# Optimization experiments

Measured on AMD Instinct MI355X. Metric: run time of the kernel, lower is better.

The kernel has to match this reference:

```python
import jax, jax.numpy as jnp
import numpy as np

# Model config (matches init_kwargs)
B, T, D = 2, 2048, 2048
H, KH, F = 16, 4, 8192
HD = D // H            # 128
G = H // KH            # q heads per kv head = 4
EPS = 1e-5


def _ln(x, g, b):
    m = jnp.mean(x, axis=-1, keepdims=True)
    v = jnp.mean((x - m) ** 2, axis=-1, keepdims=True)
    return (x - m) * jax.lax.rsqrt(v + EPS) * g + b


def setup_inputs() -> dict:
    key = jax.random.key(0)
    ks = jax.random.split(key, 8)

    def xav(k, shape):
        lim = (6.0 / (shape[0] + shape[1])) ** 0.5
        return jax.random.uniform(k, shape, jnp.float32, -lim, lim)

    x = jax.random.normal(ks[0], (B, T, D), jnp.float32)
    mask = jnp.tril(jnp.ones((1, 1, T, T), jnp.int32))  # causal
    # Linear weights stored as [in, out] (transpose of torch nn.Linear)
    return {
        "x": x,
        "mask": mask,
        "Wq": xav(ks[1], (D, H * HD)), "bq": jnp.zeros((H * HD,), jnp.float32),
        "Wk": xav(ks[2], (D, KH * HD)), "bk": jnp.zeros((KH * HD,), jnp.float32),
        "Wv": xav(ks[3], (D, KH * HD)), "bv": jnp.zeros((KH * HD,), jnp.float32),
        "Wo": xav(ks[4], (H * HD, D)), "bo": jnp.zeros((D,), jnp.float32),
        "ln1_g": jnp.ones((D,), jnp.float32), "ln1_b": jnp.zeros((D,), jnp.float32),
        "ln2_g": jnp.ones((D,), jnp.float32), "ln2_b": jnp.zeros((D,), jnp.float32),
        "fln_g": jnp.ones((D,), jnp.float32), "fln_b": jnp.zeros((D,), jnp.float32),
        "W1": xav(ks[5], (D, F)), "b1": jnp.zeros((F,), jnp.float32),
        "W2": xav(ks[6], (D, F)), "b2": jnp.zeros((F,), jnp.float32),
        "W3": xav(ks[7], (F, D)), "b3": jnp.zeros((D,), jnp.float32),
    }


def reference(x, mask, Wq, bq, Wk, bk, Wv, bv, Wo, bo,
              ln1_g, ln1_b, ln2_g, ln2_b, fln_g, fln_b,
              W1, b1, W2, b2, W3, b3):
    scale = 1.0 / np.sqrt(HD)
    # --- attention block (pre-LN + residual) ---
    h = _ln(x, ln1_g, ln1_b)
    q = (h @ Wq + bq).reshape(B, T, KH, G, HD)   # q head k*G+g uses kv head k
    k = (h @ Wk + bk).reshape(B, T, KH, HD)
    v = (h @ Wv + bv).reshape(B, T, KH, HD)
    # GQA scores without repeat_interleave: broadcast kv head across group g
    scores = jnp.einsum('btkgd,bskd->bkgts', q, k) * scale  # [B,KH,G,T,T]
    scores = jnp.clip(scores, -100.0, 100.0)
    scores = jnp.where(mask[:, :, None] == 0, -jnp.inf, scores)
    attn = jax.nn.softmax(scores, axis=-1)
    ctx = jnp.einsum('bkgts,bskd->btkgd', attn, v).reshape(B, T, H * HD)
    x = x + (ctx @ Wo + bo)  # dropout is identity in eval
    # --- ln2 then SwiGLU FFN (which has its own internal LN and residual
    # around the *post-ln2* activation, faithful to original) ---
    x = _ln(x, ln2_g, ln2_b)
    r = x
    h2 = _ln(x, fln_g, fln_b)
    g_pre = h2 @ W1 + b1
    gate = g_pre * jax.nn.sigmoid(jnp.clip(g_pre, -10.0, 10.0))
    hidden = h2 @ W2 + b2
    return r + ((gate * hidden) @ W3 + b3)
```

## Files before the change

kernel.cpp:

```cpp
#include <hip/hip_runtime.h>
#include <math.h>
#include <stdint.h>

typedef __bf16 bf16_t;
typedef __bf16 bf16x4 __attribute__((ext_vector_type(4)));
typedef __bf16 bf16x8 __attribute__((ext_vector_type(8)));
typedef float  f32x4  __attribute__((ext_vector_type(4)));

#define D_MODEL 2048
#define T_SEQ   2048
#define BATCH   2
#define NROWS   (BATCH*T_SEQ)
#define NHEAD   16
#define HDIM    128
#define KVH     4
#define KVD     (KVH*HDIM)
#define FDIM    8192
#define QKVN    3072

__device__ __forceinline__ bf16x8 mk8(bf16x4 lo, bf16x4 hi) {
  union { bf16x4 h[2]; bf16x8 v; } u;
  u.h[0] = lo; u.h[1] = hi; return u.v;
}

__device__ __forceinline__ void gl16(const bf16_t* g, bf16_t* l) {
  __builtin_amdgcn_global_load_lds(
      (const uint32_t __attribute__((address_space(1)))*)g,
      (uint32_t __attribute__((address_space(3)))*)l, 16, 0, 0);
}

__global__ __launch_bounds__(256)
void transpose_w(const float* __restrict__ in, bf16_t* __restrict__ outT, int K, int N)
{
  __shared__ __align__(16) bf16_t t[64][72];
  const int tid = threadIdx.x;
  const int k0 = blockIdx.y * 64, n0 = blockIdx.x * 64;
  const int tr = tid >> 4, tc = (tid & 15) * 4;
#pragma unroll
  for (int i = 0; i < 4; ++i) {
    f32x4 v = *(const f32x4*)(in + (size_t)(k0 + tr + 16 * i) * N + n0 + tc);
#pragma unroll
    for (int e = 0; e < 4; ++e) t[tr + 16 * i][tc + e] = (bf16_t)v[e];
  }
  __syncthreads();
#pragma unroll
  for (int s = 0; s < 2; ++s) {
    const int c = s * 256 + tid;
    const int n = c >> 3, c8 = (c & 7) * 8;
    bf16x8 o;
#pragma unroll
    for (int e = 0; e < 8; ++e) o[e] = t[c8 + e][n];
    *(bf16x8*)(outT + (size_t)(n0 + n) * K + k0 + c8) = o;
  }
}

__global__ __launch_bounds__(256)
void concat_bias(const float* __restrict__ a, const float* __restrict__ b,
                 const float* __restrict__ c, float* __restrict__ dst)
{
  const int i = blockIdx.x * 256 + threadIdx.x;
  if (i >= QKVN) return;
  dst[i] = (i < 2048) ? a[i] : (i < 2560) ? b[i - 2048] : c[i - 2560];
}

template<typename TI>
__global__ __launch_bounds__(256)
void ln_kernel(const TI* __restrict__ x, const float* __restrict__ g,
               const float* __restrict__ b, bf16_t* __restrict__ out)
{
  const int row = blockIdx.x;
  const int tid = threadIdx.x;
  const TI* xr = x + (size_t)row * D_MODEL;
  float vals[8];
  if constexpr (sizeof(TI) == 4) {
    f32x4 v0 = *(const f32x4*)(xr + tid * 8);
    f32x4 v1 = *(const f32x4*)(xr + tid * 8 + 4);
#pragma unroll
    for (int e = 0; e < 4; ++e) { vals[e] = v0[e]; vals[4 + e] = v1[e]; }
  } else {
    bf16x8 v = *(const bf16x8*)(xr + tid * 8);
#pragma unroll
    for (int e = 0; e < 8; ++e) vals[e] = (float)v[e];
  }
  float s = 0.f, s2 = 0.f;
#pragma unroll
  for (int e = 0; e < 8; ++e) { s += vals[e]; s2 += vals[e] * vals[e]; }
#pragma unroll
  for (int off = 1; off < 64; off <<= 1) { s += __shfl_xor(s, off); s2 += __shfl_xor(s2, off); }
  __shared__ float red[8];
  const int wid = tid >> 6, lane = tid & 63;
  if (lane == 0) { red[wid] = s; red[4 + wid] = s2; }
  __syncthreads();
  s  = red[0] + red[1] + red[2] + red[3];
  s2 = red[4] + red[5] + red[6] + red[7];
  const float mean = s * (1.f / D_MODEL);
  const float var  = s2 * (1.f / D_MODEL) - mean * mean;
  const float rstd = rsqrtf(var + 1e-5f);
  f32x4 g0 = *(const f32x4*)(g + tid * 8), g1 = *(const f32x4*)(g + tid * 8 + 4);
  f32x4 b0 = *(const f32x4*)(b + tid * 8), b1 = *(const f32x4*)(b + tid * 8 + 4);
  bf16x8 o;
#pragma unroll
  for (int e = 0; e < 4; ++e) {
    o[e]     = (bf16_t)((vals[e]     - mean) * rstd * g0[e] + b0[e]);
    o[4 + e] = (bf16_t)((vals[4 + e] - mean) * rstd * g1[e] + b1[e]);
  }
  *(bf16x8*)(out + (size_t)row * D_MODEL + tid * 8) = o;
}

__global__ __launch_bounds__(256)
void ln2_fused(const bf16_t* __restrict__ x, const float* __restrict__ g2,
               const float* __restrict__ b2, const float* __restrict__ gf,
               const float* __restrict__ bf_, bf16_t* __restrict__ rout,
               bf16_t* __restrict__ hout)
{
  const int row = blockIdx.x;
  const int tid = threadIdx.x;
  const int wid = tid >> 6, lane = tid & 63;
  __shared__ float red[8];
  const bf16_t* xr = x + (size_t)row * D_MODEL;
  bf16x8 v = *(const bf16x8*)(xr + tid * 8);
  float vals[8]; float s = 0.f, s2 = 0.f;
#pragma unroll
  for (int e = 0; e < 8; ++e) { vals[e] = (float)v[e]; s += vals[e]; s2 += vals[e] * vals[e]; }
#pragma unroll
  for (int off = 1; off < 64; off <<= 1) { s += __shfl_xor(s, off); s2 += __shfl_xor(s2, off); }
  if (lane == 0) { red[wid] = s; red[4 + wid] = s2; }
  __syncthreads();
  s  = red[0] + red[1] + red[2] + red[3];
  s2 = red[4] + red[5] + red[6] + red[7];
  float mean = s * (1.f / D_MODEL);
  float var  = s2 * (1.f / D_MODEL) - mean * mean;
  float rstd = rsqrtf(var + 1e-5f);
  f32x4 ga0 = *(const f32x4*)(g2 + tid * 8), ga1 = *(const f32x4*)(g2 + tid * 8 + 4);
  f32x4 ba0 = *(const f32x4*)(b2 + tid * 8), ba1 = *(const f32x4*)(b2 + tid * 8 + 4);
  float y[8];
#pragma unroll
  for (int e = 0; e < 4; ++e) {
    y[e]     = (vals[e]     - mean) * rstd * ga0[e] + ba0[e];
    y[4 + e] = (vals[4 + e] - mean) * rstd * ga1[e] + ba1[e];
  }
  bf16x8 o1;
#pragma unroll
  for (int e = 0; e < 8; ++e) o1[e] = (bf16_t)y[e];
  *(bf16x8*)(rout + (size_t)row * D_MODEL + tid * 8) = o1;
  s = 0.f; s2 = 0.f;
#pragma unroll
  for (int e = 0; e < 8; ++e) { s += y[e]; s2 += y[e] * y[e]; }
#pragma unroll
  for (int off = 1; off < 64; off <<= 1) { s += __shfl_xor(s, off); s2 += __shfl_xor(s2, off); }
  __syncthreads();
  if (lane == 0) { red[wid] = s; red[4 + wid] = s2; }
  __syncthreads();
  s  = red[0] + red[1] + red[2] + red[3];
  s2 = red[4] + red[5] + red[6] + red[7];
  mean = s * (1.f / D_MODEL);
  var  = s2 * (1.f / D_MODEL) - mean * mean;
  rstd = rsqrtf(var + 1e-5f);
  f32x4 gb0 = *(const f32x4*)(gf + tid * 8), gb1 = *(const f32x4*)(gf + tid * 8 + 4);
  f32x4 bb0 = *(const f32x4*)(bf_ + tid * 8), bb1 = *(const f32x4*)(bf_ + tid * 8 + 4);
  bf16x8 o2;
#pragma unroll
  for (int e = 0; e < 4; ++e) {
    o2[e]     = (bf16_t)((y[e]     - mean) * rstd * gb0[e] + bb0[e]);
    o2[4 + e] = (bf16_t)((y[4 + e] - mean) * rstd * gb1[e] + bb1[e]);
  }
  *(bf16x8*)(hout + (size_t)row * D_MODEL + tid * 8) = o2;
}

enum { EPI_NONE = 0, EPI_RES = 1, EPI_SILU = 2, EPI_MUL = 3 };

__device__ __forceinline__ void xcd_swz(int BMv, int BNv, int& m0, int& n0) {
  const int nbx = gridDim.x, nwg = nbx * gridDim.y;
  int flat = blockIdx.y * nbx + blockIdx.x;
  flat = (flat & 7) * (nwg >> 3) + (flat >> 3);
  m0 = (flat / nbx) * BMv; n0 = (flat % nbx) * BNv;
}

template<int EPI, int BM_T, typename TE, typename TO>
__global__ __launch_bounds__(512, 2)
void gemm8p(const bf16_t* __restrict__ A, const bf16_t* __restrict__ Bt,
            const float* __restrict__ bias, const TE* __restrict__ extra,
            TO* __restrict__ out, int M, int N, int K)
{
  constexpr int ALs = BM_T / 128;
  constexpr int RF  = BM_T / 32;
  __shared__ __align__(16) bf16_t As[2][2][BM_T * 32];
  __shared__ __align__(16) bf16_t Bs[2][2][256 * 32];
  const int tid = threadIdx.x, lane = tid & 63, wid = tid >> 6;
  const int wr = wid >> 2, wc = wid & 3;
  const int l16 = lane & 15, lq = lane >> 4;
  int m0, n0; xcd_swz(BM_T, 256, m0, n0);

  const bf16_t* aP[ALs]; int aL[ALs];
#pragma unroll
  for (int s = 0; s < ALs; ++s) {
    const int c = s * 512 + tid;
    const int row = c >> 2, pos = c & 3;
    aP[s] = A + (size_t)(m0 + row) * K + (pos ^ ((row >> 1) & 3)) * 8;
    aL[s] = (s * 512 + wid * 64) * 8;
  }
  const bf16_t* bP[2]; int bL[2];
#pragma unroll
  for (int s = 0; s < 2; ++s) {
    const int c = s * 512 + tid;
    const int row = c >> 2, pos = c & 3;
    bP[s] = Bt + (size_t)(n0 + row) * K + (pos ^ ((row >> 1) & 3)) * 8;
    bL[s] = (s * 512 + wid * 64) * 8;
  }

  int offA[RF];
#pragma unroll
  for (int i = 0; i < RF; ++i) {
    const int r = wr * (BM_T / 2) + i * 16 + l16;
    offA[i] = r * 32 + ((lq ^ ((r >> 1) & 3)) * 8);
  }
  int offB[4];
#pragma unroll
  for (int jj = 0; jj < 4; ++jj) {
    const int r = wc * 64 + jj * 16 + l16;
    offB[jj] = r * 32 + ((lq ^ ((r >> 1) & 3)) * 8);
  }

  f32x4 acc[RF][4];
#pragma unroll
  for (int i = 0; i < RF; ++i)
#pragma unroll
    for (int j = 0; j < 4; ++j) acc[i][j] = (f32x4){0.f, 0.f, 0.f, 0.f};

  auto SA = [&](int t, int bb, int kh) {
#pragma unroll
    for (int s = 0; s < ALs; ++s) gl16(aP[s] + t * 64 + kh * 32, &As[bb][kh][aL[s]]);
  };
  auto SB = [&](int t, int bb, int kh) {
#pragma unroll
    for (int s = 0; s < 2; ++s) gl16(bP[s] + t * 64 + kh * 32, &Bs[bb][kh][bL[s]]);
  };
#define BAR_()  __builtin_amdgcn_s_barrier()
#define LGKM_() do { asm volatile("s_waitcnt lgkmcnt(0)" ::: "memory"); \
                     __builtin_amdgcn_sched_barrier(0); } while (0)

  const int nt = K >> 6;
  SA(0, 0, 0); SB(0, 0, 0); SA(0, 0, 1); SB(0, 0, 1);
  if (nt > 1) { SA(1, 1, 0); SB(1, 1, 0); SA(1, 1, 1); }
  if (nt > 2) {
    if constexpr (ALs == 2) asm volatile("s_waitcnt vmcnt(6)" ::: "memory");
    else                    asm volatile("s_waitcnt vmcnt(4)" ::: "memory");
  } else {
    asm volatile("s_waitcnt vmcnt(0)" ::: "memory");
  }
  BAR_();

  for (int t = 0; t < nt; ++t) {
    const int b = t & 1, ob = b ^ 1;
    const bool s1 = (t + 1 < nt), s2 = (t + 2 < nt);
    bf16x8 af[RF], bf0, bf1;
#pragma unroll
    for (int i = 0; i < RF; ++i) af[i] = *(const bf16x8*)(&As[b][0][offA[i]]);
    bf0 = *(const bf16x8*)(&Bs[b][0][offB[0]]);
    bf1 = *(const bf16x8*)(&Bs[b][0][offB[1]]);
    if (s1) SB(t + 1, ob, 1);
    BAR_(); LGKM_();
    __builtin_amdgcn_s_setprio(1);
#pragma unroll
    for (int i = 0; i < RF; ++i) {
      acc[i][0] = __builtin_amdgcn_mfma_f32_16x16x32_bf16(af[i], bf0, acc[i][0], 0, 0, 0);
      acc[i][1] = __builtin_amdgcn_mfma_f32_16x16x32_bf16(af[i], bf1, acc[i][1], 0, 0, 0);
    }
    __builtin_amdgcn_s_setprio(0);
    BAR_();
    bf0 = *(const bf16x8*)(&Bs[b][0][offB[2]]);
    bf1 = *(const bf16x8*)(&Bs[b][0][offB[3]]);
    if (s2) SA(t + 2, b, 0);
    BAR_(); LGKM_();
    __builtin_amdgcn_s_setprio(1);
#pragma unroll
    for (int i = 0; i < RF; ++i) {
      acc[i][2] = __builtin_amdgcn_mfma_f32_16x16x32_bf16(af[i], bf0, acc[i][2], 0, 0, 0);
      acc[i][3] = __builtin_amdgcn_mfma_f32_16x16x32_bf16(af[i], bf1, acc[i][3], 0, 0, 0);
    }
    __builtin_amdgcn_s_setprio(0);
    BAR_();
#pragma unroll
    for (int i = 0; i < RF; ++i) af[i] = *(const bf16x8*)(&As[b][1][offA[i]]);
    bf0 = *(const bf16x8*)(&Bs[b][1][offB[0]]);
    bf1 = *(const bf16x8*)(&Bs[b][1][offB[1]]);
    if (s2) SB(t + 2, b, 0);
    BAR_(); LGKM_();
    __builtin_amdgcn_s_setprio(1);
#pragma unroll
    for (int i = 0; i < RF; ++i) {
      acc[i][0] = __builtin_amdgcn_mfma_f32_16x16x32_bf16(af[i], bf0, acc[i][0], 0, 0, 0);
      acc[i][1] = __builtin_amdgcn_mfma_f32_16x16x32_bf16(af[i], bf1, acc[i][1], 0, 0, 0);
    }
    __builtin_amdgcn_s_setprio(0);
    BAR_();
    bf0 = *(const bf16x8*)(&Bs[b][1][offB[2]]);
    bf1 = *(const bf16x8*)(&Bs[b][1][offB[3]]);
    if (s2) SA(t + 2, b, 1);
    BAR_(); LGKM_();
    __builtin_amdgcn_s_setprio(1);
#pragma unroll
    for (int i = 0; i < RF; ++i) {
      acc[i][2] = __builtin_amdgcn_mfma_f32_16x16x32_bf16(af[i], bf0, acc[i][2], 0, 0, 0);
      acc[i][3] = __builtin_amdgcn_mfma_f32_16x16x32_bf16(af[i], bf1, acc[i][3], 0, 0, 0);
    }
    __builtin_amdgcn_s_setprio(0);
    if (t < nt - 2) {
      if constexpr (ALs == 2) asm volatile("s_waitcnt vmcnt(6)" ::: "memory");
      else                    asm volatile("s_waitcnt vmcnt(4)" ::: "memory");
    } else {
      asm volatile("s_waitcnt vmcnt(0)" ::: "memory");
    }
    BAR_();
  }

  if constexpr (sizeof(TO) == 2) {
    float* sc = (float*)(&As[0][0][0]) + (size_t)wid * (16 * 72);
    const int rr = lane >> 3, cc8 = (lane & 7) * 8;
#pragma unroll
    for (int i = 0; i < RF; ++i) {
      const int row0 = m0 + wr * (BM_T / 2) + i * 16;
#pragma unroll
      for (int j = 0; j < 4; ++j) {
        const float bb = bias[n0 + wc * 64 + j * 16 + l16];
#pragma unroll
        for (int e = 0; e < 4; ++e) {
          float vv = acc[i][j][e] + bb;
          if (EPI == EPI_SILU) { float c2 = fminf(fmaxf(vv, -10.f), 10.f); vv = vv / (1.f + __expf(-c2)); }
          sc[(lq * 4 + e) * 72 + j * 16 + l16] = vv;
        }
      }
      asm volatile("s_waitcnt lgkmcnt(0)" ::: "memory");
      __builtin_amdgcn_sched_barrier(0);
#pragma unroll
      for (int q = 0; q < 2; ++q) {
        const int row = row0 + rr + q * 8;
        const size_t base = (size_t)row * N + n0 + wc * 64 + cc8;
        f32x4 a0 = *(const f32x4*)(sc + (rr + q * 8) * 72 + cc8);
        f32x4 a1 = *(const f32x4*)(sc + (rr + q * 8) * 72 + cc8 + 4);
        bf16x8 o;
        if constexpr (EPI == EPI_RES) {
          if constexpr (sizeof(TE) == 4) {
            f32x4 x0 = *(const f32x4*)((const float*)extra + base);
            f32x4 x1 = *(const f32x4*)((const float*)extra + base + 4);
#pragma unroll
            for (int e = 0; e < 4; ++e) { o[e] = (bf16_t)(a0[e] + x0[e]); o[4 + e] = (bf16_t)(a1[e] + x1[e]); }
          } else {
            bf16x8 x8 = *(const bf16x8*)((const bf16_t*)extra + base);
#pragma unroll
            for (int e = 0; e < 4; ++e) { o[e] = (bf16_t)(a0[e] + (float)x8[e]); o[4 + e] = (bf16_t)(a1[e] + (float)x8[4 + e]); }
          }
        } else if constexpr (EPI == EPI_MUL) {
          bf16x8 x8 = *(const bf16x8*)((const bf16_t*)extra + base);
#pragma unroll
          for (int e = 0; e < 4; ++e) { o[e] = (bf16_t)(a0[e] * (float)x8[e]); o[4 + e] = (bf16_t)(a1[e] * (float)x8[4 + e]); }
        } else {
#pragma unroll
          for (int e = 0; e < 4; ++e) { o[e] = (bf16_t)a0[e]; o[4 + e] = (bf16_t)a1[e]; }
        }
        *(bf16x8*)((bf16_t*)out + base) = o;
      }
      asm volatile("s_waitcnt lgkmcnt(0)" ::: "memory");
      __builtin_amdgcn_sched_barrier(0);
    }
  } else {
#pragma unroll
    for (int j = 0; j < 4; ++j) {
      const int col = n0 + wc * 64 + j * 16 + l16;
      const float bb = bias[col];
#pragma unroll
      for (int i = 0; i < RF; ++i) {
        const int row0 = m0 + wr * (BM_T / 2) + i * 16 + lq * 4;
#pragma unroll
        for (int e = 0; e < 4; ++e) {
          const size_t idx = (size_t)(row0 + e) * N + col;
          float vv = acc[i][j][e] + bb;
          if (EPI == EPI_RES)       vv += (float)extra[idx];
          else if (EPI == EPI_SILU) { float c2 = fminf(fmaxf(vv, -10.f), 10.f); vv = vv / (1.f + __expf(-c2)); }
          else if (EPI == EPI_MUL)  vv *= (float)extra[idx];
          out[idx] = (TO)vv;
        }
      }
    }
  }
#undef BAR_
#undef LGKM_
}

template<int EPI, typename TE, typename TO>
__global__ __launch_bounds__(256, 4)
void gemm3b(const bf16_t* __restrict__ A, const bf16_t* __restrict__ Bt,
            const float* __restrict__ bias, const TE* __restrict__ extra,
            TO* __restrict__ out, int M, int N, int K)
{
  __shared__ __align__(16) bf16_t As[3][128 * 32];
  __shared__ __align__(16) bf16_t Bs[3][128 * 32];
  const int tid = threadIdx.x, lane = tid & 63, wid = tid >> 6;
  const int wr = wid >> 1, wc = wid & 1;
  const int l16 = lane & 15, lq = lane >> 4;
  int m0, n0; xcd_swz(128, 128, m0, n0);

  const bf16_t* aP[2]; const bf16_t* bP[2]; int sL[2];
#pragma unroll
  for (int s = 0; s < 2; ++s) {
    const int c = s * 256 + tid;
    const int row = c >> 2, pos = c & 3;
    const int g = pos ^ ((row >> 1) & 3);
    aP[s] = A  + (size_t)(m0 + row) * K + g * 8;
    bP[s] = Bt + (size_t)(n0 + row) * K + g * 8;
    sL[s] = (s * 256 + wid * 64) * 8;
  }

  int offA[4], offB[4];
#pragma unroll
  for (int i = 0; i < 4; ++i) {
    const int r = wr * 64 + i * 16 + l16;
    offA[i] = r * 32 + ((lq ^ ((r >> 1) & 3)) * 8);
  }
#pragma unroll
  for (int j = 0; j < 4; ++j) {
    const int r = wc * 64 + j * 16 + l16;
    offB[j] = r * 32 + ((lq ^ ((r >> 1) & 3)) * 8);
  }

  f32x4 acc[4][4];
#pragma unroll
  for (int i = 0; i < 4; ++i)
#pragma unroll
    for (int j = 0; j < 4; ++j) acc[i][j] = (f32x4){0.f, 0.f, 0.f, 0.f};

  auto STAGE = [&](int t, int b) {
    gl16(aP[0] + t * 32, &As[b][sL[0]]);
    gl16(aP[1] + t * 32, &As[b][sL[1]]);
    gl16(bP[0] + t * 32, &Bs[b][sL[0]]);
    gl16(bP[1] + t * 32, &Bs[b][sL[1]]);
  };

  const int nt = K >> 5;
  STAGE(0, 0);
  STAGE(1, 1);
  if (nt > 1) asm volatile("s_waitcnt vmcnt(4)" ::: "memory");
  else        asm volatile("s_waitcnt vmcnt(0)" ::: "memory");
  __builtin_amdgcn_s_barrier();

  int b = 0;
  for (int t = 0; t < nt; ++t) {
    bf16x8 af[4], bfr[4];
#pragma unroll
    for (int i = 0; i < 4; ++i) af[i]  = *(const bf16x8*)(&As[b][offA[i]]);
#pragma unroll
    for (int j = 0; j < 4; ++j) bfr[j] = *(const bf16x8*)(&Bs[b][offB[j]]);
    if (t + 2 < nt) {
      STAGE(t + 2, (b + 2) % 3);
      asm volatile("s_waitcnt vmcnt(4)" ::: "memory");
    } else {
      asm volatile("s_waitcnt vmcnt(0)" ::: "memory");
    }
    __builtin_amdgcn_s_barrier();
    asm volatile("s_waitcnt lgkmcnt(0)" ::: "memory");
    __builtin_amdgcn_sched_barrier(0);
    __builtin_amdgcn_s_setprio(1);
#pragma unroll
    for (int i = 0; i < 4; ++i)
#pragma unroll
      for (int j = 0; j < 4; ++j)
        acc[i][j] = __builtin_amdgcn_mfma_f32_16x16x32_bf16(af[i], bfr[j], acc[i][j], 0, 0, 0);
    __builtin_amdgcn_s_setprio(0);
    __builtin_amdgcn_s_barrier();
    b = (b + 1) % 3;
  }

  if constexpr (sizeof(TO) == 2) {
    float* sc = (float*)(&As[0][0]) + (size_t)wid * (16 * 72);
    const int rr = lane >> 3, cc8 = (lane & 7) * 8;
#pragma unroll
    for (int i = 0; i < 4; ++i) {
      const int row0 = m0 + wr * 64 + i * 16;
#pragma unroll
      for (int j = 0; j < 4; ++j) {
        const float bb = bias[n0 + wc * 64 + j * 16 + l16];
#pragma unroll
        for (int e = 0; e < 4; ++e) {
          float vv = acc[i][j][e] + bb;
          if (EPI == EPI_SILU) { float c2 = fminf(fmaxf(vv, -10.f), 10.f); vv = vv / (1.f + __expf(-c2)); }
          sc[(lq * 4 + e) * 72 + j * 16 + l16] = vv;
        }
      }
      asm volatile("s_waitcnt lgkmcnt(0)" ::: "memory");
      __builtin_amdgcn_sched_barrier(0);
#pragma unroll
      for (int q = 0; q < 2; ++q) {
        const int row = row0 + rr + q * 8;
        const size_t base = (size_t)row * N + n0 + wc * 64 + cc8;
        f32x4 a0 = *(const f32x4*)(sc + (rr + q * 8) * 72 + cc8);
        f32x4 a1 = *(const f32x4*)(sc + (rr + q * 8) * 72 + cc8 + 4);
        bf16x8 o;
        if constexpr (EPI == EPI_RES) {
          if constexpr (sizeof(TE) == 4) {
            f32x4 x0 = *(const f32x4*)((const float*)extra + base);
            f32x4 x1 = *(const f32x4*)((const float*)extra + base + 4);
#pragma unroll
            for (int e = 0; e < 4; ++e) { o[e] = (bf16_t)(a0[e] + x0[e]); o[4 + e] = (bf16_t)(a1[e] + x1[e]); }
          } else {
            bf16x8 x8 = *(const bf16x8*)((const bf16_t*)extra + base);
#pragma unroll
            for (int e = 0; e < 4; ++e) { o[e] = (bf16_t)(a0[e] + (float)x8[e]); o[4 + e] = (bf16_t)(a1[e] + (float)x8[4 + e]); }
          }
        } else if constexpr (EPI == EPI_MUL) {
          bf16x8 x8 = *(const bf16x8*)((const bf16_t*)extra + base);
#pragma unroll
          for (int e = 0; e < 4; ++e) { o[e] = (bf16_t)(a0[e] * (float)x8[e]); o[4 + e] = (bf16_t)(a1[e] * (float)x8[4 + e]); }
        } else {
#pragma unroll
          for (int e = 0; e < 4; ++e) { o[e] = (bf16_t)a0[e]; o[4 + e] = (bf16_t)a1[e]; }
        }
        *(bf16x8*)((bf16_t*)out + base) = o;
      }
      asm volatile("s_waitcnt lgkmcnt(0)" ::: "memory");
      __builtin_amdgcn_sched_barrier(0);
    }
  } else {
#pragma unroll
    for (int j = 0; j < 4; ++j) {
      const int col = n0 + wc * 64 + j * 16 + l16;
      const float bb = bias[col];
#pragma unroll
      for (int i = 0; i < 4; ++i) {
        const int row0 = m0 + wr * 64 + i * 16 + lq * 4;
#pragma unroll
        for (int e = 0; e < 4; ++e) {
          const size_t idx = (size_t)(row0 + e) * N + col;
          float vv = acc[i][j][e] + bb;
          if (EPI == EPI_RES)       vv += (float)extra[idx];
          else if (EPI == EPI_SILU) { float c2 = fminf(fmaxf(vv, -10.f), 10.f); vv = vv / (1.f + __expf(-c2)); }
          else if (EPI == EPI_MUL)  vv *= (float)extra[idx];
          out[idx] = (TO)vv;
        }
      }
    }
  }
}

template<int EPI, typename TE, typename TO>
__global__ __launch_bounds__(256)
void gemm_kernel(const bf16_t* __restrict__ A, const float* __restrict__ W,
                 const float* __restrict__ bias, const TE* __restrict__ extra,
                 TO* __restrict__ out, int M, int N, int K)
{
  __shared__ bf16_t As[128][40];
  __shared__ bf16_t Bs[128][40];
  const int tid  = threadIdx.x;
  const int lane = tid & 63, wid = tid >> 6;
  const int wr = wid >> 1, wc = wid & 1;
  const int l16 = lane & 15, lq = lane >> 4;
  const int m0 = blockIdx.y * 128, n0 = blockIdx.x * 128;

  f32x4 acc[4][4];
#pragma unroll
  for (int i = 0; i < 4; ++i)
#pragma unroll
    for (int j = 0; j < 4; ++j) acc[i][j] = (f32x4){0.f, 0.f, 0.f, 0.f};

  const int ar = tid >> 1, ah = tid & 1;
  const int kk = tid & 31, cc = tid >> 5;

  for (int k0 = 0; k0 < K; k0 += 32) {
    const bf16_t* asrc = A + (size_t)(m0 + ar) * K + k0 + ah * 16;
    *(bf16x8*)(&As[ar][ah * 16])     = *(const bf16x8*)(asrc);
    *(bf16x8*)(&As[ar][ah * 16 + 8]) = *(const bf16x8*)(asrc + 8);
    const float* wsrc = W + (size_t)(k0 + kk) * N + n0;
#pragma unroll
    for (int it = 0; it < 2; ++it) {
      const int c = cc * 8 + it * 64;
      f32x4 wa = *(const f32x4*)(wsrc + c);
      f32x4 wb = *(const f32x4*)(wsrc + c + 4);
#pragma unroll
      for (int e = 0; e < 4; ++e) {
        Bs[c + e][kk]     = (bf16_t)wa[e];
        Bs[c + 4 + e][kk] = (bf16_t)wb[e];
      }
    }
    __syncthreads();
    bf16x8 af[4], bfr[4];
#pragma unroll
    for (int i = 0; i < 4; ++i) {
      const bf16_t* p = &As[wr * 64 + i * 16 + l16][lq * 4];
      af[i] = mk8(*(const bf16x4*)p, *(const bf16x4*)(p + 16));
    }
#pragma unroll
    for (int j = 0; j < 4; ++j) {
      const bf16_t* p = &Bs[wc * 64 + j * 16 + l16][lq * 4];
      bfr[j] = mk8(*(const bf16x4*)p, *(const bf16x4*)(p + 16));
    }
#pragma unroll
    for (int i = 0; i < 4; ++i)
#pragma unroll
      for (int j = 0; j < 4; ++j)
        acc[i][j] = __builtin_amdgcn_mfma_f32_16x16x32_bf16(af[i], bfr[j], acc[i][j], 0, 0, 0);
    __syncthreads();
  }

#pragma unroll
  for (int j = 0; j < 4; ++j) {
    const int col = n0 + wc * 64 + j * 16 + l16;
    const float bb = bias[col];
#pragma unroll
    for (int i = 0; i < 4; ++i) {
      const int row0 = m0 + wr * 64 + i * 16 + lq * 4;
#pragma unroll
      for (int e = 0; e < 4; ++e) {
        const size_t idx = (size_t)(row0 + e) * N + col;
        float vv = acc[i][j][e] + bb;
        if (EPI == EPI_RES)       vv += (float)extra[idx];
        else if (EPI == EPI_SILU) { float c2 = fminf(fmaxf(vv, -10.f), 10.f); vv = vv / (1.f + __expf(-c2)); }
        else if (EPI == EPI_MUL)  vv *= (float)extra[idx];
        out[idx] = (TO)vv;
      }
    }
  }
}

__global__ __launch_bounds__(512)
void attn_kernel(const bf16_t* __restrict__ q, const bf16_t* __restrict__ k,
                 const bf16_t* __restrict__ v, bf16_t* __restrict__ ctx,
                 int q_ld, int kv_ld)
{
  __shared__ __align__(16) bf16_t Ks[2][64 * 128];
  __shared__ __align__(16) bf16_t Vt[128][72];

  const int tid = threadIdx.x, lane = tid & 63, wid = tid >> 6;
  const int l16 = lane & 15, lq = lane >> 4;
  const int bh = blockIdx.y;
  const int b = bh >> 4, h = bh & 15;
  const int kh = h >> 2;
  const float scale = 0.08838834764831845f;

  const int vr = tid & 63, vo = (tid >> 6) * 8;

  for (int pass = 0; pass < 2; ++pass) {
    const int qt = pass ? blockIdx.x : (15 - blockIdx.x);
    const int qbase = qt * 128;
    const int qrow = qbase + wid * 16 + l16;

    const bf16_t* qp = q + (size_t)(b * T_SEQ + qrow) * q_ld + h * HDIM;
    bf16x8 bq[4];
#pragma unroll
    for (int s = 0; s < 4; ++s) bq[s] = *(const bf16x8*)(qp + s * 32 + lq * 8);

    float m_r = -1e30f, l_r = 0.f;
    f32x4 acc_o[8];
#pragma unroll
    for (int jh = 0; jh < 8; ++jh) acc_o[jh] = (f32x4){0.f, 0.f, 0.f, 0.f};

    const int ntiles = (qbase + 128) >> 6;

    bf16x8 vregs[2];
#pragma unroll
    for (int it = 0; it < 2; ++it) {
      const int c = it * 512 + tid;
      const int kvr = c >> 4, pos = c & 15;
      gl16(k + (size_t)(b * T_SEQ + kvr) * kv_ld + kh * HDIM + (pos ^ (kvr & 7)) * 8,
           &Ks[0][(it * 512 + wid * 64) * 8]);
    }
#pragma unroll
    for (int it = 0; it < 2; ++it)
      vregs[it] = *(const bf16x8*)(v + (size_t)(b * T_SEQ + vr) * kv_ld + kh * HDIM + vo + it * 64);

    int cur = 0;
    for (int t = 0; t < ntiles; ++t) {
      const int kb = t * 64;
#pragma unroll
      for (int it = 0; it < 2; ++it) {
#pragma unroll
        for (int e = 0; e < 8; ++e) Vt[vo + it * 64 + e][vr] = vregs[it][e];
      }
      if (t + 1 < ntiles) {
        const int kb2 = kb + 64;
#pragma unroll
        for (int it = 0; it < 2; ++it) {
          const int c = it * 512 + tid;
          const int kvr = c >> 4, pos = c & 15;
          gl16(k + (size_t)(b * T_SEQ + kb2 + kvr) * kv_ld + kh * HDIM + (pos ^ (kvr & 7)) * 8,
               &Ks[cur ^ 1][(it * 512 + wid * 64) * 8]);
        }
#pragma unroll
        for (int it = 0; it < 2; ++it)
          vregs[it] = *(const bf16x8*)(v + (size_t)(b * T_SEQ + kb2 + vr) * kv_ld + kh * HDIM + vo + it * 64);
      }
      asm volatile("s_waitcnt lgkmcnt(0)" ::: "memory");
      __builtin_amdgcn_s_barrier();
      __builtin_amdgcn_sched_barrier(0);

      f32x4 sf[4];
#pragma unroll
      for (int j = 0; j < 4; ++j) {
        sf[j] = (f32x4){0.f, 0.f, 0.f, 0.f};
        const int kvr = j * 16 + l16;
#pragma unroll
        for (int s = 0; s < 4; ++s) {
          bf16x8 ak = *(const bf16x8*)(&Ks[cur][kvr * 128 + (((s * 4 + lq) ^ (kvr & 7)) * 8)]);
          sf[j] = __builtin_amdgcn_mfma_f32_16x16x32_bf16(ak, bq[s], sf[j], 0, 0, 0);
        }
      }

      float p[4][4];
      float tmax = -1e30f;
#pragma unroll
      for (int j = 0; j < 4; ++j)
#pragma unroll
        for (int e = 0; e < 4; ++e) {
          const int kvc = kb + j * 16 + lq * 4 + e;
          float sv = sf[j][e] * scale;
          sv = fminf(fmaxf(sv, -100.f), 100.f);
          if (kvc > qrow) sv = -1e30f;
          p[j][e] = sv;
          tmax = fmaxf(tmax, sv);
        }
      tmax = fmaxf(tmax, __shfl_xor(tmax, 16));
      tmax = fmaxf(tmax, __shfl_xor(tmax, 32));
      const float mnew = fmaxf(m_r, tmax);
      const float resc = __expf(m_r - mnew);
      m_r = mnew;
      float rsum = 0.f;
#pragma unroll
      for (int j = 0; j < 4; ++j)
#pragma unroll
        for (int e = 0; e < 4; ++e) {
          p[j][e] = __expf(p[j][e] - m_r);
          rsum += p[j][e];
        }
      rsum += __shfl_xor(rsum, 16);
      rsum += __shfl_xor(rsum, 32);
      l_r = l_r * resc + rsum;

      float resc4[4];
#pragma unroll
      for (int e = 0; e < 4; ++e) resc4[e] = __shfl(resc, lq * 4 + e);
#pragma unroll
      for (int jh = 0; jh < 8; ++jh)
#pragma unroll
        for (int e = 0; e < 4; ++e) acc_o[jh][e] *= resc4[e];

      bf16x8 pa[2];
#pragma unroll
      for (int sk = 0; sk < 2; ++sk) {
        bf16x4 lo, hi;
#pragma unroll
        for (int e = 0; e < 4; ++e) { lo[e] = (bf16_t)p[2 * sk][e]; hi[e] = (bf16_t)p[2 * sk + 1][e]; }
        pa[sk] = mk8(lo, hi);
      }
#pragma unroll
      for (int jh = 0; jh < 8; ++jh) {
#pragma unroll
        for (int sk = 0; sk < 2; ++sk) {
          const bf16_t* pV = &Vt[jh * 16 + l16][sk * 32 + lq * 4];
          bf16x8 bv2 = mk8(*(const bf16x4*)pV, *(const bf16x4*)(pV + 16));
          acc_o[jh] = __builtin_amdgcn_mfma_f32_16x16x32_bf16(pa[sk], bv2, acc_o[jh], 0, 0, 0);
        }
      }
      __builtin_amdgcn_s_barrier();
      cur ^= 1;
    }

    float l4[4];
#pragma unroll
    for (int e = 0; e < 4; ++e) l4[e] = __shfl(l_r, lq * 4 + e);
    bf16_t* op = ctx + (size_t)(b * T_SEQ + qbase + wid * 16) * D_MODEL + h * HDIM;
#pragma unroll
    for (int jh = 0; jh < 8; ++jh)
#pragma unroll
      for (int e = 0; e < 4; ++e)
        op[(size_t)(lq * 4 + e) * D_MODEL + jh * 16 + l16] = (bf16_t)(acc_o[jh][e] / l4[e]);
  }
}

extern "C" void kernel_launch(void* const* d_in, const int* in_sizes, int n_in,
                              void* d_out, int out_size, void* d_ws, size_t ws_size,
                              hipStream_t stream)
{
  const float* x   = (const float*)d_in[0];
  const float* Wq  = (const float*)d_in[2];
  const float* bq  = (const float*)d_in[3];
  const float* Wk  = (const float*)d_in[4];
  const float* bk  = (const float*)d_in[5];
  const float* Wv  = (const float*)d_in[6];
  const float* bv  = (const float*)d_in[7];
  const float* Wo  = (const float*)d_in[8];
  const float* bo  = (const float*)d_in[9];
  const float* g1  = (const float*)d_in[10];
  const float* b1n = (const float*)d_in[11];
  const float* g2  = (const float*)d_in[12];
  const float* b2n = (const float*)d_in[13];
  const float* gf  = (const float*)d_in[14];
  const float* bfn = (const float*)d_in[15];
  const float* W1  = (const float*)d_in[16];
  const float* bb1 = (const float*)d_in[17];
  const float* W2  = (const float*)d_in[18];
  const float* bb2 = (const float*)d_in[19];
  const float* W3  = (const float*)d_in[20];
  const float* bb3 = (const float*)d_in[21];
  float* out = (float*)d_out;

  char* ws = (char*)d_ws;
  size_t off = 0;
  auto alloc = [&](size_t bytes) -> void* {
    void* p = ws + off; off += (bytes + 255) & ~(size_t)255; return p;
  };
  const dim3 blk(256);

  bf16_t* Wt_qkv = (bf16_t*)alloc((size_t)QKVN * D_MODEL * 2);
  bf16_t* Wt_o   = (bf16_t*)alloc((size_t)D_MODEL * D_MODEL * 2);
  bf16_t* Wt1    = (bf16_t*)alloc((size_t)FDIM * D_MODEL * 2);
  bf16_t* Wt2    = (bf16_t*)alloc((size_t)FDIM * D_MODEL * 2);
  bf16_t* Wt3    = (bf16_t*)alloc((size_t)D_MODEL * FDIM * 2);
  float*  bqkv   = (float*)alloc((size_t)QKVN * 4);
  bf16_t* hbuf   = (bf16_t*)alloc((size_t)NROWS * D_MODEL * 2);
  bf16_t* qkvbuf = (bf16_t*)alloc((size_t)NROWS * QKVN * 2);
  bf16_t* rbuf   = (bf16_t*)alloc((size_t)NROWS * D_MODEL * 2);
  bf16_t* h2buf  = (bf16_t*)alloc((size_t)NROWS * D_MODEL * 2);
  const size_t core = off;

  if (core <= ws_size) {
    size_t avail = ws_size - core;
    int chunk = (int)((avail / ((size_t)FDIM * 2)) & ~(size_t)255);
    bf16_t* gbuf;
    if (chunk >= 256) { gbuf = (bf16_t*)(ws + core); if (chunk > NROWS) chunk = NROWS; }
    else              { gbuf = qkvbuf; chunk = 1536; }
    bf16_t* x1buf = qkvbuf;

    transpose_w<<<dim3(32, 32),  blk, 0, stream>>>(Wq, Wt_qkv, D_MODEL, 2048);
    transpose_w<<<dim3(8, 32),   blk, 0, stream>>>(Wk, Wt_qkv + (size_t)2048 * D_MODEL, D_MODEL, 512);
    transpose_w<<<dim3(8, 32),   blk, 0, stream>>>(Wv, Wt_qkv + (size_t)2560 * D_MODEL, D_MODEL, 512);
    transpose_w<<<dim3(32, 32),  blk, 0, stream>>>(Wo, Wt_o, D_MODEL, D_MODEL);
    transpose_w<<<dim3(128, 32), blk, 0, stream>>>(W1, Wt1, D_MODEL, FDIM);
    transpose_w<<<dim3(128, 32), blk, 0, stream>>>(W2, Wt2, D_MODEL, FDIM);
    transpose_w<<<dim3(32, 128), blk, 0, stream>>>(W3, Wt3, FDIM, D_MODEL);
    concat_bias<<<12, blk, 0, stream>>>(bq, bk, bv, bqkv);

    ln_kernel<float><<<NROWS, blk, 0, stream>>>(x, g1, b1n, hbuf);
    gemm3b<EPI_NONE, bf16_t, bf16_t><<<dim3(QKVN / 128, NROWS / 128), blk, 0, stream>>>(
        hbuf, Wt_qkv, bqkv, nullptr, qkvbuf, NROWS, QKVN, D_MODEL);
    attn_kernel<<<dim3(8, 32), 512, 0, stream>>>(
        qkvbuf, qkvbuf + 2048, qkvbuf + 2560, hbuf, QKVN, QKVN);
    gemm3b<EPI_RES, float, bf16_t><<<dim3(D_MODEL / 128, NROWS / 128), blk, 0, stream>>>(
        hbuf, Wt_o, bo, x, x1buf, NROWS, D_MODEL, D_MODEL);
    ln2_fused<<<NROWS, blk, 0, stream>>>(x1buf, g2, b2n, gf, bfn, rbuf, h2buf);

    for (int r0 = 0; r0 < NROWS; r0 += chunk) {
      const int rows = (NROWS - r0 < chunk) ? (NROWS - r0) : chunk;
      gemm8p<EPI_SILU, 256, bf16_t, bf16_t><<<dim3(FDIM / 256, rows / 256), 512, 0, stream>>>(
          h2buf + (size_t)r0 * D_MODEL, Wt1, bb1, nullptr, gbuf, rows, FDIM, D_MODEL);
      gemm8p<EPI_MUL, 256, bf16_t, bf16_t><<<dim3(FDIM / 256, rows / 256), 512, 0, stream>>>(
          h2buf + (size_t)r0 * D_MODEL, Wt2, bb2, gbuf, gbuf, rows, FDIM, D_MODEL);
      gemm3b<EPI_RES, bf16_t, float><<<dim3(D_MODEL / 128, rows / 128), blk, 0, stream>>>(
          gbuf, Wt3, bb3, rbuf + (size_t)r0 * D_MODEL, out + (size_t)r0 * D_MODEL, rows, D_MODEL, FDIM);
    }
    return;
  }

  off = 0;
  const size_t DBYTES = (size_t)NROWS * D_MODEL * 2;
  bf16_t* fhbuf  = (bf16_t*)alloc(DBYTES);
  bf16_t* fqbuf  = (bf16_t*)alloc(DBYTES);
  bf16_t* fkbuf  = (bf16_t*)alloc((size_t)NROWS * KVD * 2);
  bf16_t* fvbuf  = (bf16_t*)alloc((size_t)NROWS * KVD * 2);
  bf16_t* frbuf  = (bf16_t*)alloc(DBYTES);
  bf16_t* fh2buf = (bf16_t*)alloc(DBYTES);
  const size_t base = off;
  size_t avail = (ws_size > base) ? (ws_size - base) : 0;
  int chunk = (int)((avail / ((size_t)FDIM * 2)) & ~(size_t)127);
  bf16_t* gbuf;
  if (chunk >= 128) { gbuf = (bf16_t*)(ws + base); if (chunk > NROWS) chunk = NROWS; }
  else              { gbuf = fqbuf; chunk = 1024; }

  ln_kernel<float><<<NROWS, blk, 0, stream>>>(x, g1, b1n, fhbuf);
  gemm_kernel<EPI_NONE, bf16_t, bf16_t><<<dim3(16, 32), blk, 0, stream>>>(fhbuf, Wq, bq, nullptr, fqbuf, NROWS, 2048, 2048);
  gemm_kernel<EPI_NONE, bf16_t, bf16_t><<<dim3(4, 32),  blk, 0, stream>>>(fhbuf, Wk, bk, nullptr, fkbuf, NROWS, 512, 2048);
  gemm_kernel<EPI_NONE, bf16_t, bf16_t><<<dim3(4, 32),  blk, 0, stream>>>(fhbuf, Wv, bv, nullptr, fvbuf, NROWS, 512, 2048);
  attn_kernel<<<dim3(8, 32), 512, 0, stream>>>(fqbuf, fkbuf, fvbuf, fhbuf, 2048, 512);
  gemm_kernel<EPI_RES, float, bf16_t><<<dim3(16, 32), blk, 0, stream>>>(fhbuf, Wo, bo, x, fqbuf, NROWS, 2048, 2048);
  ln_kernel<bf16_t><<<NROWS, blk, 0, stream>>>(fqbuf, g2, b2n, frbuf);
  ln_kernel<bf16_t><<<NROWS, blk, 0, stream>>>(frbuf, gf, bfn, fh2buf);
  for (int r0 = 0; r0 < NROWS; r0 += chunk) {
    const int rows = (NROWS - r0 < chunk) ? (NROWS - r0) : chunk;
    gemm_kernel<EPI_SILU, bf16_t, bf16_t><<<dim3(64, rows / 128), blk, 0, stream>>>(
        fh2buf + (size_t)r0 * D_MODEL, W1, bb1, nullptr, gbuf, rows, FDIM, 2048);
    gemm_kernel<EPI_MUL, bf16_t, bf16_t><<<dim3(64, rows / 128), blk, 0, stream>>>(
        fh2buf + (size_t)r0 * D_MODEL, W2, bb2, gbuf, gbuf, rows, FDIM, 2048);
    gemm_kernel<EPI_RES, bf16_t, float><<<dim3(16, rows / 128), blk, 0, stream>>>(
        gbuf, W3, bb3, frbuf + (size_t)r0 * D_MODEL, out + (size_t)r0 * D_MODEL, rows, 2048, FDIM);
  }
}
```

Measured before the change: 752.0 us.

## Fuse W1 and W2 FFN GEMMs into one dual-accumulator SwiGLU kernel

```diff
diff --git a/kernel.cpp b/kernel.cpp
--- a/kernel.cpp
+++ b/kernel.cpp
@@ -176,215 +176,170 @@
   m0 = (flat / nbx) * BMv; n0 = (flat % nbx) * BNv;
 }
 
-template<int EPI, int BM_T, typename TE, typename TO>
 __global__ __launch_bounds__(512, 2)
-void gemm8p(const bf16_t* __restrict__ A, const bf16_t* __restrict__ Bt,
-            const float* __restrict__ bias, const TE* __restrict__ extra,
-            TO* __restrict__ out, int M, int N, int K)
+void gemm_w12f(const bf16_t* __restrict__ A, const bf16_t* __restrict__ B1t,
+               const bf16_t* __restrict__ B2t, const float* __restrict__ bias1,
+               const float* __restrict__ bias2, bf16_t* __restrict__ out,
+               int M, int N, int K)
 {
-  constexpr int ALs = BM_T / 128;
-  constexpr int RF  = BM_T / 32;
-  __shared__ __align__(16) bf16_t As[2][2][BM_T * 32];
-  __shared__ __align__(16) bf16_t Bs[2][2][256 * 32];
+  __shared__ __align__(16) bf16_t As[2][2][256 * 32];
+  __shared__ __align__(16) bf16_t B1s[2][2][128 * 32];
+  __shared__ __align__(16) bf16_t B2s[2][2][128 * 32];
   const int tid = threadIdx.x, lane = tid & 63, wid = tid >> 6;
   const int wr = wid >> 2, wc = wid & 3;
   const int l16 = lane & 15, lq = lane >> 4;
-  int m0, n0; xcd_swz(BM_T, 256, m0, n0);
-
-  const bf16_t* aP[ALs]; int aL[ALs];
-#pragma unroll
-  for (int s = 0; s < ALs; ++s) {
+  int m0, n0; xcd_swz(256, 128, m0, n0);
+
+  const bf16_t* aP[2]; int aL[2];
+#pragma unroll
+  for (int s = 0; s < 2; ++s) {
     const int c = s * 512 + tid;
     const int row = c >> 2, pos = c & 3;
     aP[s] = A + (size_t)(m0 + row) * K + (pos ^ ((row >> 1) & 3)) * 8;
     aL[s] = (s * 512 + wid * 64) * 8;
   }
-  const bf16_t* bP[2]; int bL[2];
-#pragma unroll
-  for (int s = 0; s < 2; ++s) {
-    const int c = s * 512 + tid;
-    const int row = c >> 2, pos = c & 3;
-    bP[s] = Bt + (size_t)(n0 + row) * K + (pos ^ ((row >> 1) & 3)) * 8;
-    bL[s] = (s * 512 + wid * 64) * 8;
-  }
-
-  int offA[RF];
-#pragma unroll
-  for (int i = 0; i < RF; ++i) {
-    const int r = wr * (BM_T / 2) + i * 16 + l16;
+  const bf16_t* b1P; const bf16_t* b2P; int bL;
+  {
+    const int row = tid >> 2, pos = tid & 3;
+    const int g = pos ^ ((row >> 1) & 3);
+    b1P = B1t + (size_t)(n0 + row) * K + g * 8;
+    b2P = B2t + (size_t)(n0 + row) * K + g * 8;
+    bL = (wid * 64) * 8;
+  }
+
+  int offA[8];
+#pragma unroll
+  for (int i = 0; i < 8; ++i) {
+    const int r = wr * 128 + i * 16 + l16;
     offA[i] = r * 32 + ((lq ^ ((r >> 1) & 3)) * 8);
   }
-  int offB[4];
-#pragma unroll
-  for (int jj = 0; jj < 4; ++jj) {
-    const int r = wc * 64 + jj * 16 + l16;
+  int offB[2];
+#pragma unroll
+  for (int jj = 0; jj < 2; ++jj) {
+    const int r = wc * 32 + jj * 16 + l16;
     offB[jj] = r * 32 + ((lq ^ ((r >> 1) & 3)) * 8);
   }
 
-  f32x4 acc[RF][4];
-#pragma unroll
-  for (int i = 0; i < RF; ++i)
-#pragma unroll
-    for (int j = 0; j < 4; ++j) acc[i][j] = (f32x4){0.f, 0.f, 0.f, 0.f};
+  f32x4 acc1[8][2], acc2[8][2];
+#pragma unroll
+  for (int i = 0; i < 8; ++i)
+#pragma unroll
+    for (int j = 0; j < 2; ++j) {
+      acc1[i][j] = (f32x4){0.f, 0.f, 0.f, 0.f};
+      acc2[i][j] = (f32x4){0.f, 0.f, 0.f, 0.f};
+    }
 
   auto SA = [&](int t, int bb, int kh) {
 #pragma unroll
-    for (int s = 0; s < ALs; ++s) gl16(aP[s] + t * 64 + kh * 32, &As[bb][kh][aL[s]]);
+    for (int s = 0; s < 2; ++s) gl16(aP[s] + t * 64 + kh * 32, &As[bb][kh][aL[s]]);
   };
-  auto SB = [&](int t, int bb, int kh) {
-#pragma unroll
-    for (int s = 0; s < 2; ++s) gl16(bP[s] + t * 64 + kh * 32, &Bs[bb][kh][bL[s]]);
+  auto SB12 = [&](int t, int bb, int kh) {
+    gl16(b1P + t * 64 + kh * 32, &B1s[bb][kh][bL]);
+    gl16(b2P + t * 64 + kh * 32, &B2s[bb][kh][bL]);
   };
 #define BAR_()  __builtin_amdgcn_s_barrier()
 #define LGKM_() do { asm volatile("s_waitcnt lgkmcnt(0)" ::: "memory"); \
                      __builtin_amdgcn_sched_barrier(0); } while (0)
 
   const int nt = K >> 6;
-  SA(0, 0, 0); SB(0, 0, 0); SA(0, 0, 1); SB(0, 0, 1);
-  if (nt > 1) { SA(1, 1, 0); SB(1, 1, 0); SA(1, 1, 1); }
-  if (nt > 2) {
-    if constexpr (ALs == 2) asm volatile("s_waitcnt vmcnt(6)" ::: "memory");
-    else                    asm volatile("s_waitcnt vmcnt(4)" ::: "memory");
-  } else {
-    asm volatile("s_waitcnt vmcnt(0)" ::: "memory");
-  }
+  SA(0, 0, 0); SB12(0, 0, 0); SA(0, 0, 1); SB12(0, 0, 1);
+  if (nt > 1) { SA(1, 1, 0); SB12(1, 1, 0); SA(1, 1, 1); }
+  if (nt > 2) asm volatile("s_waitcnt vmcnt(6)" ::: "memory");
+  else        asm volatile("s_waitcnt vmcnt(0)" ::: "memory");
   BAR_();
 
   for (int t = 0; t < nt; ++t) {
     const int b = t & 1, ob = b ^ 1;
     const bool s1 = (t + 1 < nt), s2 = (t + 2 < nt);
-    bf16x8 af[RF], bf0, bf1;
-#pragma unroll
-    for (int i = 0; i < RF; ++i) af[i] = *(const bf16x8*)(&As[b][0][offA[i]]);
-    bf0 = *(const bf16x8*)(&Bs[b][0][offB[0]]);
-    bf1 = *(const bf16x8*)(&Bs[b][0][offB[1]]);
-    if (s1) SB(t + 1, ob, 1);
+    bf16x8 af[8], bf0, bf1;
+#pragma unroll
+    for (int i = 0; i < 8; ++i) af[i] = *(const bf16x8*)(&As[b][0][offA[i]]);
+    bf0 = *(const bf16x8*)(&B1s[b][0][offB[0]]);
+    bf1 = *(const bf16x8*)(&B1s[b][0][offB[1]]);
+    if (s1) SB12(t + 1, ob, 1);
     BAR_(); LGKM_();
     __builtin_amdgcn_s_setprio(1);
 #pragma unroll
-    for (int i = 0; i < RF; ++i) {
-      acc[i][0] = __builtin_amdgcn_mfma_f32_16x16x32_bf16(af[i], bf0, acc[i][0], 0, 0, 0);
-      acc[i][1] = __builtin_amdgcn_mfma_f32_16x16x32_bf16(af[i], bf1, acc[i][1], 0, 0, 0);
+    for (int i = 0; i < 8; ++i) {
+      acc1[i][0] = __builtin_amdgcn_mfma_f32_16x16x32_bf16(af[i], bf0, acc1[i][0], 0, 0, 0);
+      acc1[i][1] = __builtin_amdgcn_mfma_f32_16x16x32_bf16(af[i], bf1, acc1[i][1], 0, 0, 0);
     }
     __builtin_amdgcn_s_setprio(0);
     BAR_();
-    bf0 = *(const bf16x8*)(&Bs[b][0][offB[2]]);
-    bf1 = *(const bf16x8*)(&Bs[b][0][offB[3]]);
+    bf0 = *(const bf16x8*)(&B2s[b][0][offB[0]]);
+    bf1 = *(const bf16x8*)(&B2s[b][0][offB[1]]);
     if (s2) SA(t + 2, b, 0);
     BAR_(); LGKM_();
     __builtin_amdgcn_s_setprio(1);
 #pragma unroll
-    for (int i = 0; i < RF; ++i) {
-      acc[i][2] = __builtin_amdgcn_mfma_f32_16x16x32_bf16(af[i], bf0, acc[i][2], 0, 0, 0);
-      acc[i][3] = __builtin_amdgcn_mfma_f32_16x16x32_bf16(af[i], bf1, acc[i][3], 0, 0, 0);
+    for (int i = 0; i < 8; ++i) {
+      acc2[i][0] = __builtin_amdgcn_mfma_f32_16x16x32_bf16(af[i], bf0, acc2[i][0], 0, 0, 0);
+      acc2[i][1] = __builtin_amdgcn_mfma_f32_16x16x32_bf16(af[i], bf1, acc2[i][1], 0, 0, 0);
     }
     __builtin_amdgcn_s_setprio(0);
     BAR_();
 #pragma unroll
-    for (int i = 0; i < RF; ++i) af[i] = *(const bf16x8*)(&As[b][1][offA[i]]);
-    bf0 = *(const bf16x8*)(&Bs[b][1][offB[0]]);
-    bf1 = *(const bf16x8*)(&Bs[b][1][offB[1]]);
-    if (s2) SB(t + 2, b, 0);
+    for (int i = 0; i < 8; ++i) af[i] = *(const bf16x8*)(&As[b][1][offA[i]]);
+    bf0 = *(const bf16x8*)(&B1s[b][1][offB[0]]);
+    bf1 = *(const bf16x8*)(&B1s[b][1][offB[1]]);
+    if (s2) SB12(t + 2, b, 0);
     BAR_(); LGKM_();
     __builtin_amdgcn_s_setprio(1);
 #pragma unroll
-    for (int i = 0; i < RF; ++i) {
-      acc[i][0] = __builtin_amdgcn_mfma_f32_16x16x32_bf16(af[i], bf0, acc[i][0], 0, 0, 0);
-      acc[i][1] = __builtin_amdgcn_mfma_f32_16x16x32_bf16(af[i], bf1, acc[i][1], 0, 0, 0);
+    for (int i = 0; i < 8; ++i) {
+      acc1[i][0] = __builtin_amdgcn_mfma_f32_16x16x32_bf16(af[i], bf0, acc1[i][0], 0, 0, 0);
+      acc1[i][1] = __builtin_amdgcn_mfma_f32_16x16x32_bf16(af[i], bf1, acc1[i][1], 0, 0, 0);
     }
     __builtin_amdgcn_s_setprio(0);
     BAR_();
-    bf0 = *(const bf16x8*)(&Bs[b][1][offB[2]]);
-    bf1 = *(const bf16x8*)(&Bs[b][1][offB[3]]);
+    bf0 = *(const bf16x8*)(&B2s[b][1][offB[0]]);
+    bf1 = *(const bf16x8*)(&B2s[b][1][offB[1]]);
     if (s2) SA(t + 2, b, 1);
     BAR_(); LGKM_();
     __builtin_amdgcn_s_setprio(1);
 #pragma unroll
-    for (int i = 0; i < RF; ++i) {
-      acc[i][2] = __builtin_amdgcn_mfma_f32_16x16x32_bf16(af[i], bf0, acc[i][2], 0, 0, 0);
-      acc[i][3] = __builtin_amdgcn_mfma_f32_16x16x32_bf16(af[i], bf1, acc[i][3], 0, 0, 0);
+    for (int i = 0; i < 8; ++i) {
+      acc2[i][0] = __builtin_amdgcn_mfma_f32_16x16x32_bf16(af[i], bf0, acc2[i][0], 0, 0, 0);
+      acc2[i][1] = __builtin_amdgcn_mfma_f32_16x16x32_bf16(af[i], bf1, acc2[i][1], 0, 0, 0);
     }
     __builtin_amdgcn_s_setprio(0);
-    if (t < nt - 2) {
-      if constexpr (ALs == 2) asm volatile("s_waitcnt vmcnt(6)" ::: "memory");
-      else                    asm volatile("s_waitcnt vmcnt(4)" ::: "memory");
-    } else {
-      asm volatile("s_waitcnt vmcnt(0)" ::: "memory");
-    }
+    if (t < nt - 2) asm volatile("s_waitcnt vmcnt(6)" ::: "memory");
+    else            asm volatile("s_waitcnt vmcnt(0)" ::: "memory");
     BAR_();
-  }
-
-  if constexpr (sizeof(TO) == 2) {
-    float* sc = (float*)(&As[0][0][0]) + (size_t)wid * (16 * 72);
-    const int rr = lane >> 3, cc8 = (lane & 7) * 8;
-#pragma unroll
-    for (int i = 0; i < RF; ++i) {
-      const int row0 = m0 + wr * (BM_T / 2) + i * 16;
-#pragma unroll
-      for (int j = 0; j < 4; ++j) {
-        const float bb = bias[n0 + wc * 64 + j * 16 + l16];
-#pragma unroll
-        for (int e = 0; e < 4; ++e) {
-          float vv = acc[i][j][e] + bb;
-          if (EPI == EPI_SILU) { float c2 = fminf(fmaxf(vv, -10.f), 10.f); vv = vv / (1.f + __expf(-c2)); }
-          sc[(lq * 4 + e) * 72 + j * 16 + l16] = vv;
-        }
-      }
-      asm volatile("s_waitcnt lgkmcnt(0)" ::: "memory");
-      __builtin_amdgcn_sched_barrier(0);
-#pragma unroll
-      for (int q = 0; q < 2; ++q) {
-        const int row = row0 + rr + q * 8;
-        const size_t base = (size_t)row * N + n0 + wc * 64 + cc8;
-        f32x4 a0 = *(const f32x4*)(sc + (rr + q * 8) * 72 + cc8);
-        f32x4 a1 = *(const f32x4*)(sc + (rr + q * 8) * 72 + cc8 + 4);
-        bf16x8 o;
-        if constexpr (EPI == EPI_RES) {
-          if constexpr (sizeof(TE) == 4) {
-            f32x4 x0 = *(const f32x4*)((const float*)extra + base);
-            f32x4 x1 = *(const f32x4*)((const float*)extra + base + 4);
-#pragma unroll
-            for (int e = 0; e < 4; ++e) { o[e] = (bf16_t)(a0[e] + x0[e]); o[4 + e] = (bf16_t)(a1[e] + x1[e]); }
-          } else {
-            bf16x8 x8 = *(const bf16x8*)((const bf16_t*)extra + base);
-#pragma unroll
-            for (int e = 0; e < 4; ++e) { o[e] = (bf16_t)(a0[e] + (float)x8[e]); o[4 + e] = (bf16_t)(a1[e] + (float)x8[4 + e]); }
-          }
-        } else if constexpr (EPI == EPI_MUL) {
-          bf16x8 x8 = *(const bf16x8*)((const bf16_t*)extra + base);
-#pragma unroll
-          for (int e = 0; e < 4; ++e) { o[e] = (bf16_t)(a0[e] * (float)x8[e]); o[4 + e] = (bf16_t)(a1[e] * (float)x8[4 + e]); }
-        } else {
-#pragma unroll
-          for (int e = 0; e < 4; ++e) { o[e] = (bf16_t)a0[e]; o[4 + e] = (bf16_t)a1[e]; }
-        }
-        *(bf16x8*)((bf16_t*)out + base) = o;
-      }
-      asm volatile("s_waitcnt lgkmcnt(0)" ::: "memory");
-      __builtin_amdgcn_sched_barrier(0);
-    }
-  } else {
-#pragma unroll
-    for (int j = 0; j < 4; ++j) {
-      const int col = n0 + wc * 64 + j * 16 + l16;
-      const float bb = bias[col];
-#pragma unroll
-      for (int i = 0; i < RF; ++i) {
-        const int row0 = m0 + wr * (BM_T / 2) + i * 16 + lq * 4;
-#pragma unroll
-        for (int e = 0; e < 4; ++e) {
-          const size_t idx = (size_t)(row0 + e) * N + col;
-          float vv = acc[i][j][e] + bb;
-          if (EPI == EPI_RES)       vv += (float)extra[idx];
-          else if (EPI == EPI_SILU) { float c2 = fminf(fmaxf(vv, -10.f), 10.f); vv = vv / (1.f + __expf(-c2)); }
-          else if (EPI == EPI_MUL)  vv *= (float)extra[idx];
-          out[idx] = (TO)vv;
-        }
-      }
-    }
   }
 #undef BAR_
 #undef LGKM_
+
+  float* sc = (float*)(&As[0][0][0]) + (size_t)wid * (16 * 40);
+  const int rr = lane >> 2, c8 = (lane & 3) * 8;
+#pragma unroll
+  for (int i = 0; i < 8; ++i) {
+    const int row0 = m0 + wr * 128 + i * 16;
+#pragma unroll
+    for (int j = 0; j < 2; ++j) {
+      const int col = n0 + wc * 32 + j * 16 + l16;
+      const float bb1 = bias1[col], bb2 = bias2[col];
+#pragma unroll
+      for (int e = 0; e < 4; ++e) {
+        float g = acc1[i][j][e] + bb1;
+        float h = acc2[i][j][e] + bb2;
+        float c2 = fminf(fmaxf(g, -10.f), 10.f);
+        sc[(lq * 4 + e) * 40 + j * 16 + l16] = (g / (1.f + __expf(-c2))) * h;
+      }
+    }
+    asm volatile("s_waitcnt lgkmcnt(0)" ::: "memory");
+    __builtin_amdgcn_sched_barrier(0);
+    {
+      f32x4 a0 = *(const f32x4*)(sc + rr * 40 + c8);
+      f32x4 a1 = *(const f32x4*)(sc + rr * 40 + c8 + 4);
+      bf16x8 o;
+#pragma unroll
+      for (int e = 0; e < 4; ++e) { o[e] = (bf16_t)a0[e]; o[4 + e] = (bf16_t)a1[e]; }
+      *(bf16x8*)(out + (size_t)(row0 + rr) * N + n0 + wc * 32 + c8) = o;
+    }
+    asm volatile("s_waitcnt lgkmcnt(0)" ::: "memory");
+    __builtin_amdgcn_sched_barrier(0);
+  }
 }
 
 template<int EPI, typename TE, typename TO>
@@ -848,10 +803,8 @@
 
     for (int r0 = 0; r0 < NROWS; r0 += chunk) {
       const int rows = (NROWS - r0 < chunk) ? (NROWS - r0) : chunk;
-      gemm8p<EPI_SILU, 256, bf16_t, bf16_t><<<dim3(FDIM / 256, rows / 256), 512, 0, stream>>>(
-          h2buf + (size_t)r0 * D_MODEL, Wt1, bb1, nullptr, gbuf, rows, FDIM, D_MODEL);
-      gemm8p<EPI_MUL, 256, bf16_t, bf16_t><<<dim3(FDIM / 256, rows / 256), 512, 0, stream>>>(
-          h2buf + (size_t)r0 * D_MODEL, Wt2, bb2, gbuf, gbuf, rows, FDIM, D_MODEL);
+      gemm_w12f<<<dim3(FDIM / 128, rows / 256), 512, 0, stream>>>(
+          h2buf + (size_t)r0 * D_MODEL, Wt1, Wt2, bb1, bb2, gbuf, rows, FDIM, D_MODEL);
       gemm3b<EPI_RES, bf16_t, float><<<dim3(D_MODEL / 128, rows / 128), blk, 0, stream>>>(
           gbuf, Wt3, bb3, rbuf + (size_t)r0 * D_MODEL, out + (size_t)r0 * D_MODEL, rows, D_MODEL, FDIM);
     }
```

Result: no change. 757.0 us (+0.7%).
